# Optimization experiments

Hardware: AMD Instinct MI355X
Metric: run time of the kernel (lower is better)

## Reference

```python
import jax, jax.numpy as jnp
import numpy as np

D = 1024; H = 16; K = 64; BK = 32; FFN = 4096; LORA = 48; CHUNK = 64
THETA_CLIP = float(np.pi / 2)
THETA_INIT = float(np.pi / 16)


def layernorm(x, g, b, eps=1e-6):
    m = x.mean(-1, keepdims=True)
    v = ((x - m) ** 2).mean(-1, keepdims=True)
    return (x - m) * jax.lax.rsqrt(v + eps) * g + b


def setup_inputs() -> dict:
    key = jax.random.key(0)
    ks = jax.random.split(key, 24)
    w = lambda k, s: jax.random.normal(k, s, jnp.float32) * 0.02
    return {
        "x": jax.random.normal(ks[0], (4, 2048, D), jnp.float32),
        "Wq": w(ks[1], (D, D)), "bq": jnp.zeros((D,), jnp.float32),
        "Wk": w(ks[2], (D, D)), "bk": jnp.zeros((D,), jnp.float32),
        "Wv": w(ks[3], (D, D)), "bv": jnp.zeros((D,), jnp.float32),
        "Wo": w(ks[4], (D, D)), "bo": jnp.zeros((D,), jnp.float32),
        "n1g": jnp.ones((D,), jnp.float32), "n1b": jnp.zeros((D,), jnp.float32),
        "n2g": jnp.ones((D,), jnp.float32), "n2b": jnp.zeros((D,), jnp.float32),
        "theta_base": jax.random.uniform(ks[5], (H, BK), jnp.float32, -THETA_INIT, THETA_INIT),
        "theta_w1": w(ks[6], (D, LORA)),
        "theta_w2": jax.random.uniform(ks[7], (LORA, H * BK), jnp.float32, -0.01, 0.01),
        "lambda_base": jax.random.uniform(ks[8], (H, BK), jnp.float32, 0.5, 6.0),
        "eta": jax.random.normal(ks[9], (H, BK), jnp.float32) * 0.1,
        "Wf1": w(ks[10], (D, FFN)), "bf1": jnp.zeros((FFN,), jnp.float32),
        "Wf2": w(ks[11], (FFN, D)), "bf2": jnp.zeros((D,), jnp.float32),
    }


def _forward(x, Wq, bq, Wk, bk, Wv, bv, Wo, bo, n1g, n1b, n2g, n2b,
             theta_base, theta_w1, theta_w2, lambda_base, eta, Wf1, bf1, Wf2, bf2):
    B, T, _ = x.shape
    NC = T // CHUNK
    xn = layernorm(x, n1g, n1b)
    # projections -> (B, H, T, K)
    q = (xn @ Wq + bq).reshape(B, T, H, K).transpose(0, 2, 1, 3)
    k = (xn @ Wk + bk).reshape(B, T, H, K).transpose(0, 2, 1, 3)
    v = (xn @ Wv + bv).reshape(B, T, H, K).transpose(0, 2, 1, 3)
    phi_k = jnp.where(k > 0, k + 1.0, jnp.exp(k))  # elu(k) + 1
    qp = q.reshape(B, H, T, BK, 2)
    kp = phi_k.reshape(B, H, T, BK, 2)
    q_c = jax.lax.complex(qp[..., 0], qp[..., 1])  # (B,H,T,BK) complex64
    k_c = jax.lax.complex(kp[..., 0], kp[..., 1])
    # data-dependent rotation angles via LoRA
    lora = jnp.tanh(xn @ theta_w1) @ theta_w2  # (B,T,H*BK)
    theta = theta_base[None, None] + lora.reshape(B, T, H, BK)
    theta = jnp.clip(theta, -THETA_CLIP, THETA_CLIP).transpose(0, 2, 1, 3)  # (B,H,T,BK)
    lam = lambda_base[None, :, None, :] + eta[None, :, None, :] * theta ** 2
    log_z = jax.lax.complex(-lam, theta)  # complex log-decay per step

    def chunks(a):  # (B,H,T,...) -> (NC,B,H,CHUNK,...)
        return jnp.moveaxis(a.reshape(B, H, NC, CHUNK, *a.shape[3:]), 2, 0)

    tril = jnp.tril(jnp.ones((CHUNK, CHUNK), bool))[None, None, :, :, None]

    def step(c, inputs):
        lz, kc, qc, vf = inputs  # (B,H,tc,BK)x3, (B,H,tc,K)
        cumlog = jnp.cumsum(lz, axis=2)
        diff = cumlog[:, :, :, None, :] - cumlog[:, :, None, :, :]  # (B,H,tc,tc,BK)
        real = jnp.where(tril, diff.real, -60.0)
        A = jnp.where(tril, jnp.exp(jax.lax.complex(real, diff.imag)),
                      jnp.zeros((), jnp.complex64))
        scaled_k = A * kc[:, :, None, :, :]
        S_intra = jnp.einsum('bhtsk,bhsv->bhtkv', scaled_k, vf.astype(jnp.complex64))
        decay = jnp.exp(cumlog)
        S_total = decay[..., None] * c[:, :, None] + S_intra  # (B,H,tc,BK,K)
        y = jnp.einsum('bhtk,bhtkv->bhtv', jnp.conj(qc), S_total).real
        return S_total[:, :, -1], y

    c0 = jnp.zeros((B, H, BK, K), jnp.complex64)
    _, ys = jax.lax.scan(step, c0, (chunks(log_z), chunks(k_c), chunks(q_c), chunks(v)))
    out = jnp.moveaxis(ys, 0, 2).reshape(B, H, T, K)
    attn = out.transpose(0, 2, 1, 3).reshape(B, T, D) @ Wo + bo
    x1 = x + attn
    h = layernorm(x1, n2g, n2b)
    return x1 + jax.nn.gelu(h @ Wf1 + bf1) @ Wf2 + bf2


def reference(x, Wq, bq, Wk, bk, Wv, bv, Wo, bo, n1g, n1b, n2g, n2b,
              theta_base, theta_w1, theta_w2, lambda_base, eta, Wf1, bf1, Wf2, bf2):
    return _forward(x, Wq, bq, Wk, bk, Wv, bv, Wo, bo, n1g, n1b, n2g, n2b,
                    theta_base, theta_w1, theta_w2, lambda_base, eta, Wf1, bf1, Wf2, bf2)
```

## Files before the change

### kernel.cpp

```cpp
#include <hip/hip_runtime.h>


#define QS 3328

typedef __bf16 bf16x8 __attribute__((ext_vector_type(8)));
typedef float f32x4 __attribute__((ext_vector_type(4)));

__device__ __forceinline__ unsigned short f2bf(float f) {
  unsigned int u = __builtin_bit_cast(unsigned int, f);
  u += 0x7FFFu + ((u >> 16) & 1u);
  return (unsigned short)(u >> 16);
}
__device__ __forceinline__ float bf2f(unsigned short u) {
  unsigned int x = ((unsigned int)u) << 16;
  return __builtin_bit_cast(float, x);
}
__device__ __forceinline__ unsigned int pack2(float a, float b) {
  return (unsigned int)f2bf(a) | ((unsigned int)f2bf(b) << 16);
}

__device__ __forceinline__ void gload_lds16(const void* g, void* l) {
  __builtin_amdgcn_global_load_lds((const __attribute__((address_space(1))) void*)g,
                                   (__attribute__((address_space(3))) void*)l, 16, 0, 0);
}

__device__ __forceinline__ float gelu_tanh(float v) {
  const float z = 0.7978845608028654f * fmaf(0.044715f * v * v, v, v);
  const float e = __expf(2.f * z);
  return 0.5f * v * (2.f - 2.f / (1.f + e));
}

__global__ void fill_kernel(float* p, float v, int n) {
  int i = blockIdx.x * 256 + threadIdx.x;
  if (i < n) p[i] = v;
}

__global__ __launch_bounds__(256) void ln_kernel(
    const float* __restrict__ x, const float* __restrict__ g,
    const float* __restrict__ b, unsigned short* __restrict__ out) {
  const int row = blockIdx.x, tid = threadIdx.x;
  float4 v = ((const float4*)(x + (size_t)row * 1024))[tid];
  float s = v.x + v.y + v.z + v.w;
  float sq = v.x * v.x + v.y * v.y + v.z * v.z + v.w * v.w;
#pragma unroll
  for (int o = 32; o > 0; o >>= 1) { s += __shfl_xor(s, o); sq += __shfl_xor(sq, o); }
  __shared__ float red[8];
  const int wid = tid >> 6;
  if ((tid & 63) == 0) { red[wid] = s; red[4 + wid] = sq; }
  __syncthreads();
  s = red[0] + red[1] + red[2] + red[3];
  sq = red[4] + red[5] + red[6] + red[7];
  const float mean = s * (1.f / 1024.f);
  const float var = sq * (1.f / 1024.f) - mean * mean;
  const float rstd = rsqrtf(var + 1e-6f);
  float4 gv = ((const float4*)g)[tid];
  float4 bvv = ((const float4*)b)[tid];
  ushort4 o4;
  o4.x = f2bf((v.x - mean) * rstd * gv.x + bvv.x);
  o4.y = f2bf((v.y - mean) * rstd * gv.y + bvv.y);
  o4.z = f2bf((v.z - mean) * rstd * gv.z + bvv.z);
  o4.w = f2bf((v.w - mean) * rstd * gv.w + bvv.w);
  *(ushort4*)(out + (size_t)row * 1024 + tid * 4) = o4;
}

__global__ __launch_bounds__(256) void transpose_bf16(
    const float* __restrict__ src, unsigned short* __restrict__ dst, int K, int N) {
  __shared__ float tile[32][33];
  const int n0 = blockIdx.x * 32, k0 = blockIdx.y * 32;
  const int tx = threadIdx.x, ty = threadIdx.y;
#pragma unroll
  for (int j = 0; j < 32; j += 8) tile[tx][ty + j] = src[(size_t)(k0 + ty + j) * N + n0 + tx];
  __syncthreads();
#pragma unroll
  for (int j = 0; j < 32; j += 8)
    dst[(size_t)(n0 + ty + j) * K + k0 + tx] = f2bf(tile[ty + j][tx]);
}

__global__ __launch_bounds__(256) void prep_wcat(
    const float* __restrict__ Wq, const float* __restrict__ Wk,
    const float* __restrict__ Wv, const float* __restrict__ tw1,
    unsigned short* __restrict__ dst) {
  __shared__ float tile[32][33];
  const int r0 = blockIdx.x * 32, c0 = blockIdx.y * 32;
  const int tx = threadIdx.x, ty = threadIdx.y;
  const int r = r0 + tx;
#pragma unroll
  for (int j = 0; j < 32; j += 8) {
    const int c = c0 + ty + j;
    float v;
    if (r < 1024) v = Wq[(size_t)c * 1024 + r];
    else if (r < 2048) v = Wk[(size_t)c * 1024 + (r - 1024)];
    else if (r < 3072) v = Wv[(size_t)c * 1024 + (r - 2048)];
    else if (r < 3120) v = tw1[(size_t)c * 48 + (r - 3072)];
    else v = 0.f;
    tile[tx][ty + j] = v;
  }
  __syncthreads();
#pragma unroll
  for (int j = 0; j < 32; j += 8)
    dst[(size_t)(r0 + ty + j) * 1024 + c0 + tx] = f2bf(tile[ty + j][tx]);
}

__global__ void biascat_kernel(const float* bq, const float* bk, const float* bv, float* dst) {
  int i = blockIdx.x * 256 + threadIdx.x;
  if (i >= QS) return;
  float v = 0.f;
  if (i < 1024) v = bq[i];
  else if (i < 2048) v = bk[i - 1024];
  else if (i < 3072) v = bv[i - 2048];
  dst[i] = v;
}

template <int MODE>
__global__ __launch_bounds__(256) void gemm_kernel(
    const unsigned short* __restrict__ A, const unsigned short* __restrict__ BT,
    const float* __restrict__ bias, const float* __restrict__ res,
    void* __restrict__ out, int N, int Kd) {
  __shared__ unsigned short As[128 * 64];
  __shared__ unsigned short Bs[128 * 64];
  const int nwg = gridDim.x * gridDim.y;
  int d = blockIdx.y * gridDim.x + blockIdx.x;
  d = (d & 7) * (nwg >> 3) + (d >> 3);
  const int n0 = (d % gridDim.x) * 128, m0 = (d / gridDim.x) * 128;

  const int tid = threadIdx.x, wv = tid >> 6, ln = tid & 63;
  const int wm = wv >> 1, wn = wv & 1;
  const int l15 = ln & 15, hi4 = ln >> 4;
  const int rbase = wv * 8 + (ln >> 3);
  const int kgofs = ((ln & 7) ^ ((ln >> 3) & 7)) * 8;

  f32x4 acc[4][4] = {};
  for (int k0 = 0; k0 < Kd; k0 += 64) {
#pragma unroll
    for (int jj = 0; jj < 4; ++jj) {
      gload_lds16(A + (size_t)(m0 + jj * 32 + rbase) * Kd + k0 + kgofs,
                  (char*)As + (jj * 256 + wv * 64) * 16);
      gload_lds16(BT + (size_t)(n0 + jj * 32 + rbase) * Kd + k0 + kgofs,
                  (char*)Bs + (jj * 256 + wv * 64) * 16);
    }
    __syncthreads();
#pragma unroll
    for (int kk = 0; kk < 64; kk += 32) {
      const int kg = (kk >> 3) + hi4;
      bf16x8 av[4], bv[4];
#pragma unroll
      for (int f = 0; f < 4; ++f) {
        const int ra = wm * 64 + f * 16 + l15;
        const int rb2 = wn * 64 + f * 16 + l15;
        av[f] = *(const bf16x8*)&As[(ra * 8 + (kg ^ (ra & 7))) * 8];
        bv[f] = *(const bf16x8*)&Bs[(rb2 * 8 + (kg ^ (rb2 & 7))) * 8];
      }
#pragma unroll
      for (int fm = 0; fm < 4; ++fm)
#pragma unroll
        for (int fn = 0; fn < 4; ++fn)
          acc[fm][fn] = __builtin_amdgcn_mfma_f32_16x16x32_bf16(av[fm], bv[fn], acc[fm][fn], 0, 0, 0);
    }
    __syncthreads();
  }
  const int rb = hi4 * 4;
#pragma unroll
  for (int fm = 0; fm < 4; ++fm) {
#pragma unroll
    for (int fn = 0; fn < 4; ++fn) {
      const int row = m0 + wm * 64 + fm * 16 + rb;
      const int col = n0 + wn * 64 + fn * 16 + l15;
      const float bval = bias[col];
#pragma unroll
      for (int r = 0; r < 4; ++r) {
        float v = acc[fm][fn][r] + bval;
        const size_t oi = (size_t)(row + r) * N + col;
        if constexpr (MODE == 1) v += res[oi];
        ((float*)out)[oi] = v;
      }
    }
  }
}

template <int MODE>
__global__ __launch_bounds__(512, 2) void gemm8p_kernel(
    const unsigned short* __restrict__ A, const unsigned short* __restrict__ BT,
    const float* __restrict__ bias, void* __restrict__ out,
    int N, int Kstride, int Klen) {
  __shared__ __align__(16) unsigned short SA[2][2][8192];
  __shared__ __align__(16) unsigned short SB[2][2][8192];
  const int nwg = gridDim.x * gridDim.y;
  int d = blockIdx.y * gridDim.x + blockIdx.x;
  d = (d & 7) * (nwg >> 3) + (d >> 3);
  const int n0 = (d % gridDim.x) * 256, m0 = (d / gridDim.x) * 256;
  const int koff = blockIdx.z * Klen;

  const int tid = threadIdx.x, wv = tid >> 6, ln = tid & 63;
  const int wm = wv >> 2, wn = wv & 3;
  const int l15 = ln & 15, hi4 = ln >> 4;

  const unsigned short* Abase = A + (size_t)m0 * Kstride + koff;
  const unsigned short* Bbase = BT + (size_t)n0 * Kstride + koff;

  const int srow = ln >> 3;
  const int skg = (ln & 7) ^ srow;
  const unsigned short* ga00 = Abase + (size_t)((0 * 8 + wv) * 8 + srow) * Kstride + skg * 8;
  const unsigned short* ga01 = Abase + (size_t)((1 * 8 + wv) * 8 + srow) * Kstride + skg * 8;
  const unsigned short* ga10 = Abase + (size_t)(128 + (0 * 8 + wv) * 8 + srow) * Kstride + skg * 8;
  const unsigned short* ga11 = Abase + (size_t)(128 + (1 * 8 + wv) * 8 + srow) * Kstride + skg * 8;
  const unsigned short* gb00 = Bbase + (size_t)((0 * 8 + wv) * 8 + srow) * Kstride + skg * 8;
  const unsigned short* gb01 = Bbase + (size_t)((1 * 8 + wv) * 8 + srow) * Kstride + skg * 8;
  const unsigned short* gb10 = Bbase + (size_t)(128 + (0 * 8 + wv) * 8 + srow) * Kstride + skg * 8;
  const unsigned short* gb11 = Bbase + (size_t)(128 + (1 * 8 + wv) * 8 + srow) * Kstride + skg * 8;

  auto STA = [&](int pbuf) {
    gload_lds16(ga00, (char*)SA + pbuf * 32768 + wv * 1024);
    gload_lds16(ga01, (char*)SA + pbuf * 32768 + (8 + wv) * 1024);
    gload_lds16(ga10, (char*)SA + pbuf * 32768 + 16384 + wv * 1024);
    gload_lds16(ga11, (char*)SA + pbuf * 32768 + 16384 + (8 + wv) * 1024);
    ga00 += 64; ga01 += 64; ga10 += 64; ga11 += 64;
  };
  auto STB = [&](int pbuf) {
    gload_lds16(gb00, (char*)SB + pbuf * 32768 + wv * 1024);
    gload_lds16(gb01, (char*)SB + pbuf * 32768 + (8 + wv) * 1024);
    gload_lds16(gb10, (char*)SB + pbuf * 32768 + 16384 + wv * 1024);
    gload_lds16(gb11, (char*)SB + pbuf * 32768 + 16384 + (8 + wv) * 1024);
    gb00 += 64; gb01 += 64; gb10 += 64; gb11 += 64;
  };

  const int x7 = l15 & 7;
  const char* aA0 = (const char*)SA + wm * 16384 + l15 * 128 + ((hi4 ^ x7) * 16);
  const char* aA1 = (const char*)SA + wm * 16384 + l15 * 128 + (((4 + hi4) ^ x7) * 16);
  const char* aB0 = (const char*)SB + (wn >> 1) * 16384 + (wn & 1) * 8192 + l15 * 128 + ((hi4 ^ x7) * 16);
  const char* aB1 = (const char*)SB + (wn >> 1) * 16384 + (wn & 1) * 8192 + l15 * 128 + (((4 + hi4) ^ x7) * 16);

  f32x4 acc[8][4] = {};
  const int nt = Klen >> 6;

  STA(0);
  STB(0);
  STA(1);
  asm volatile("s_waitcnt vmcnt(4)" ::: "memory");
  __builtin_amdgcn_s_barrier();

#define GTILE(P, T)                                                            \
  {                                                                            \
    if ((T) + 1 < nt) STB((P) ^ 1);                                            \
    bf16x8 bfr0[4], bfr1[4];                                                   \
    _Pragma("unroll")                                                          \
    for (int fn = 0; fn < 4; ++fn) {                                           \
      bfr0[fn] = *(const bf16x8*)(aB0 + (P) * 32768 + fn * 2048);              \
      bfr1[fn] = *(const bf16x8*)(aB1 + (P) * 32768 + fn * 2048);              \
    }                                                                          \
    _Pragma("unroll")                                                          \
    for (int q = 0; q < 8; ++q) {                                              \
      bf16x8 a0 = *(const bf16x8*)(aA0 + (P) * 32768 + q * 2048);              \
      bf16x8 a1 = *(const bf16x8*)(aA1 + (P) * 32768 + q * 2048);              \
      __builtin_amdgcn_s_setprio(1);                                           \
      _Pragma("unroll")                                                        \
      for (int fn = 0; fn < 4; ++fn) {                                         \
        acc[q][fn] = __builtin_amdgcn_mfma_f32_16x16x32_bf16(a0, bfr0[fn],     \
                                                             acc[q][fn], 0, 0, 0); \
        acc[q][fn] = __builtin_amdgcn_mfma_f32_16x16x32_bf16(a1, bfr1[fn],     \
                                                             acc[q][fn], 0, 0, 0); \
      }                                                                        \
      __builtin_amdgcn_s_setprio(0);                                           \
    }                                                                          \
    __builtin_amdgcn_s_barrier();                                              \
    if ((T) + 2 < nt) STA(P);                                                  \
    if ((T) + 1 < nt) {                                                        \
      if ((T) + 2 < nt) asm volatile("s_waitcnt vmcnt(4)" ::: "memory");       \
      else              asm volatile("s_waitcnt vmcnt(0)" ::: "memory");       \
      __builtin_amdgcn_s_barrier();                                            \
    }                                                                          \
  }

  for (int t = 0; t < nt; t += 2) {
    GTILE(0, t);
    GTILE(1, t + 1);
  }
#undef GTILE

#pragma unroll
  for (int fm = 0; fm < 8; ++fm) {
#pragma unroll
    for (int fn = 0; fn < 4; ++fn) {
      const int row = m0 + wm * 128 + fm * 16 + hi4 * 4;
      const int col = n0 + wn * 64 + fn * 16 + l15;
      float bval = 0.f;
      if constexpr (MODE != 4) bval = bias[col];
#pragma unroll
      for (int r = 0; r < 4; ++r) {
        const float v = acc[fm][fn][r] + bval;
        const size_t oi = (size_t)(row + r) * N + col;
        if constexpr (MODE == 2) {
          ((unsigned short*)out)[oi] = f2bf(gelu_tanh(v));
        } else if constexpr (MODE == 3) {
          ((unsigned short*)out)[oi] = f2bf(v);
        } else {
          ((float*)out)[(size_t)blockIdx.z * 8192 * 1024 + oi] = v;
        }
      }
    }
  }
}

__global__ __launch_bounds__(256) void reduce2_kernel(
    const float* __restrict__ p0, const float* __restrict__ p1,
    const float* __restrict__ bias, const float* __restrict__ res,
    float* __restrict__ out) {
  const size_t i = ((size_t)blockIdx.x * 256 + threadIdx.x) * 4;
  float4 a = *(const float4*)&p0[i];
  float4 b = *(const float4*)&p1[i];
  float4 r = *(const float4*)&res[i];
  float4 bv = *(const float4*)&bias[i & 1023];
  float4 o;
  o.x = a.x + b.x + r.x + bv.x;
  o.y = a.y + b.y + r.y + bv.y;
  o.z = a.z + b.z + r.z + bv.z;
  o.w = a.w + b.w + r.w + bv.w;
  *(float4*)&out[i] = o;
}

__global__ __launch_bounds__(256) void lora2_kernel(
    const unsigned short* __restrict__ qkv, const float* __restrict__ w2,
    const float* __restrict__ tbase, float* __restrict__ theta) {
  __shared__ float lt[8][48];
  const int m0 = blockIdx.x * 32;
  const int tid = threadIdx.x;
  const int col = tid * 2;
  const float tb0 = tbase[col], tb1 = tbase[col + 1];
  for (int grp = 0; grp < 4; ++grp) {
    const int mg = m0 + grp * 8;
    __syncthreads();
    for (int idx = tid; idx < 384; idx += 256) {
      const int tok = idx / 48, jj = idx % 48;
      lt[tok][jj] = tanhf(bf2f(qkv[(size_t)(mg + tok) * QS + 3072 + jj]));
    }
    __syncthreads();
    float a0[8], a1[8];
#pragma unroll
    for (int tok = 0; tok < 8; ++tok) { a0[tok] = tb0; a1[tok] = tb1; }
    for (int jj = 0; jj < 48; ++jj) {
      const float2 w = *(const float2*)&w2[(size_t)jj * 512 + col];
#pragma unroll
      for (int tok = 0; tok < 8; ++tok) {
        const float l = lt[tok][jj];
        a0[tok] = fmaf(l, w.x, a0[tok]);
        a1[tok] = fmaf(l, w.y, a1[tok]);
      }
    }
    const float CL = 1.5707963267948966f;
#pragma unroll
    for (int tok = 0; tok < 8; ++tok) {
      float c0 = fminf(fmaxf(a0[tok], -CL), CL);
      float c1 = fminf(fmaxf(a1[tok], -CL), CL);
      *(float2*)&theta[(size_t)(mg + tok) * 512 + col] = make_float2(c0, c1);
    }
  }
}

__global__ __launch_bounds__(256) void attn_intra(
    const unsigned short* __restrict__ qkv, const float* __restrict__ theta,
    const float* __restrict__ lamb, const float* __restrict__ eta,
    float* __restrict__ yi, unsigned short* __restrict__ QG,
    unsigned short* __restrict__ TCG, float* __restrict__ Dg) {
  const int c = blockIdx.x, bh = blockIdx.y;
  const int b = bh >> 4, h = bh & 15;
  const int tid = threadIdx.x, wv = tid >> 6, lane = tid & 63;
  const int sc = c * 4 + wv;
  const int cid = bh * 128 + sc;
  const int mw = b * 2048 + sc * 16;

  __shared__ unsigned short QDm[4][16][64];
  __shared__ unsigned short KDm[4][16][64];
  __shared__ unsigned short KdET[4][64][32];
  __shared__ unsigned short VT[4][64][32];
  __shared__ unsigned short Gs[4][16][32];

  {
    unsigned int* kz = (unsigned int*)&KdET[wv][0][0];
    unsigned int* vz = (unsigned int*)&VT[wv][0][0];
    for (int idx = lane; idx < 512; idx += 64) {
      const int r = idx >> 3, p = (idx & 7) + 8;
      kz[r * 16 + p] = 0; vz[r * 16 + p] = 0;
    }
    unsigned int* gz = (unsigned int*)&Gs[wv][0][0];
    for (int idx = lane; idx < 128; idx += 64) {
      const int r = idx >> 3, p = (idx & 7) + 8;
      gz[r * 16 + p] = 0;
    }
  }
  for (int ss = 0; ss < 16; ++ss)
    VT[wv][lane][ss] = qkv[(size_t)(mw + ss) * QS + 2048 + h * 64 + lane];

  const int bk = lane & 31, th = lane >> 5;
  const float lb = lamb[h * 32 + bk], et = eta[h * 32 + bk];
  float L[8], Th[8], qr[8], qi[8], kr[8], ki[8];
  float runL = 0.f, runT = 0.f;
#pragma unroll
  for (int i = 0; i < 8; ++i) {
    const size_t m = (size_t)(mw + th * 8 + i);
    const float tv = theta[m * 512 + h * 32 + bk];
    const float lam = fmaf(et * tv, tv, lb);
    runL += lam; L[i] = runL;
    runT += tv;  Th[i] = runT;
    const unsigned int qp = *(const unsigned int*)&qkv[m * QS + h * 64 + 2 * bk];
    const unsigned int kp = *(const unsigned int*)&qkv[m * QS + 1024 + h * 64 + 2 * bk];
    qr[i] = bf2f((unsigned short)(qp & 0xFFFF)); qi[i] = bf2f((unsigned short)(qp >> 16));
    const float kx = bf2f((unsigned short)(kp & 0xFFFF));
    const float ky = bf2f((unsigned short)(kp >> 16));
    kr[i] = kx > 0.f ? kx + 1.f : __expf(kx);
    ki[i] = ky > 0.f ? ky + 1.f : __expf(ky);
  }
  const float oL = __shfl_xor(runL, 32), oT = __shfl_xor(runT, 32);
  const float Lm = th ? oL : runL;
  const float Tm = th ? oT : runT;
  const float Ltot = runL + oL, Ttot = runT + oT;
  const float Lbase = th ? oL : 0.f, Tbase = th ? oT : 0.f;
  float Es, Ec; __sincosf(Tm, &Es, &Ec);
  const float Ee = __expf(-Lm);
  const float Er = Ee * Ec, Ei = Ee * Es;
  float Fs, Fc; __sincosf(Ttot - Tm, &Fs, &Fc);
  const float Fe = __expf(-(Ltot - Lm));
  const float Fr = Fe * Fc, Fi = Fe * Fs;
  if (th == 0) {
    float Ds, Dc; __sincosf(Ttot, &Ds, &Dc);
    const float De = __expf(-Ltot);
    *(float2*)&Dg[((size_t)cid * 32 + bk) * 2] = make_float2(De * Dc, De * Ds);
  }
  unsigned int* qd32 = (unsigned int*)&QDm[wv][0][0];
  unsigned int* kd32 = (unsigned int*)&KDm[wv][0][0];
#pragma unroll
  for (int i = 0; i < 8; ++i) {
    const int t = th * 8 + i;
    const float Lg = Lbase + L[i], Tg = Tbase + Th[i];
    const float dm = __expf(-(Lg - Lm));
    float sn, cs; __sincosf(Tg - Tm, &sn, &cs);
    const float qmr = dm * (qr[i] * cs + qi[i] * sn);
    const float qmi = dm * (qr[i] * sn - qi[i] * cs);
    const float rd = 1.f / dm;
    const float kmr = rd * (kr[i] * cs + ki[i] * sn);
    const float kmi = rd * (ki[i] * cs - kr[i] * sn);
    const int sidx = (t * 32 + bk) ^ ((t & 7) << 2);
    qd32[sidx] = pack2(qmr, qmi);
    kd32[sidx] = pack2(kmr, -kmi);
    ((unsigned int*)QG)[(size_t)cid * 512 + t * 32 + bk] =
        pack2(qmr * Er - qmi * Ei, qmr * Ei + qmi * Er);
    const float er = kmr * Fr - kmi * Fi;
    const float ei = kmr * Fi + kmi * Fr;
    KdET[wv][bk][t] = f2bf(er);
    KdET[wv][32 + bk][t] = f2bf(ei);
  }

  const int l15 = lane & 15, hi = lane >> 4;
  const char* qb = (const char*)&QDm[wv][0][0];
  const char* kb = (const char*)&KDm[wv][0][0];
  f32x4 z = {};
  f32x4 g = z;
  {
    bf16x8 a0 = *(const bf16x8*)(qb + l15 * 128 + ((16 * hi) ^ ((l15 & 7) << 4)));
    bf16x8 b0 = *(const bf16x8*)(kb + l15 * 128 + ((16 * hi) ^ ((l15 & 7) << 4)));
    bf16x8 a1 = *(const bf16x8*)(qb + l15 * 128 + ((64 + 16 * hi) ^ ((l15 & 7) << 4)));
    bf16x8 b1 = *(const bf16x8*)(kb + l15 * 128 + ((64 + 16 * hi) ^ ((l15 & 7) << 4)));
    g = __builtin_amdgcn_mfma_f32_16x16x32_bf16(a0, b0, g, 0, 0, 0);
    g = __builtin_amdgcn_mfma_f32_16x16x32_bf16(a1, b1, g, 0, 0, 0);
  }
#pragma unroll
  for (int r = 0; r < 4; ++r) {
    const float gv = (l15 <= 4 * hi + r) ? g[r] : 0.f;
    Gs[wv][4 * hi + r][l15] = f2bf(gv);
  }
  const char* gsb = (const char*)&Gs[wv][0][0];
  const char* vtb = (const char*)&VT[wv][0][0];
  bf16x8 aG = *(const bf16x8*)(gsb + l15 * 64 + 16 * hi);
#pragma unroll
  for (int nt = 0; nt < 4; ++nt) {
    bf16x8 bV = *(const bf16x8*)(vtb + (nt * 16 + l15) * 64 + 16 * hi);
    f32x4 y = __builtin_amdgcn_mfma_f32_16x16x32_bf16(aG, bV, z, 0, 0, 0);
#pragma unroll
    for (int r = 0; r < 4; ++r)
      yi[(size_t)cid * 1024 + (4 * hi + r) * 64 + nt * 16 + l15] = y[r];
  }
  const char* keb = (const char*)&KdET[wv][0][0];
#pragma unroll
  for (int mt = 0; mt < 4; ++mt) {
    bf16x8 aT = *(const bf16x8*)(keb + (mt * 16 + l15) * 64 + 16 * hi);
#pragma unroll
    for (int nt = 0; nt < 4; ++nt) {
      bf16x8 bV = *(const bf16x8*)(vtb + (nt * 16 + l15) * 64 + 16 * hi);
      f32x4 t4 = __builtin_amdgcn_mfma_f32_16x16x32_bf16(aT, bV, z, 0, 0, 0);
#pragma unroll
      for (int r = 0; r < 4; ++r)
        TCG[(size_t)cid * 4096 + (mt * 16 + 4 * hi + r) * 64 + nt * 16 + l15] = f2bf(t4[r]);
    }
  }
}

__global__ __launch_bounds__(256) void scanB_kernel(
    const unsigned short* __restrict__ TCG, const float* __restrict__ Dg,
    unsigned int* __restrict__ CPACK) {
  const int bh = blockIdx.x & 63, g = blockIdx.x >> 6;
  const int tid = threadIdx.x;
  const int v = g * 8 + (tid >> 5), bk = tid & 31;
  const size_t base = (size_t)bh * 128;
  float Cr = 0.f, Ci = 0.f;
  float trx[4], tix[4]; float2 dx[4];
  auto LOADQ = [&](int c0, float* tr, float* ti, float2* dd) {
#pragma unroll
    for (int u = 0; u < 4; ++u) {
      const size_t cid = base + c0 + u;
      tr[u] = bf2f(TCG[cid * 4096 + bk * 64 + v]);
      ti[u] = bf2f(TCG[cid * 4096 + (32 + bk) * 64 + v]);
      dd[u] = *(const float2*)&Dg[(cid * 32 + bk) * 2];
    }
  };
  LOADQ(0, trx, tix, dx);
  for (int c0 = 0; c0 < 128; c0 += 4) {
    float tra[4], tia[4]; float2 da[4];
#pragma unroll
    for (int u = 0; u < 4; ++u) { tra[u] = trx[u]; tia[u] = tix[u]; da[u] = dx[u]; }
    if (c0 + 4 < 128) LOADQ(c0 + 4, trx, tix, dx);
#pragma unroll
    for (int u = 0; u < 4; ++u) {
      CPACK[(base + c0 + u) * 2048 + v * 32 + bk] = pack2(Cr, -Ci);
      const float nr = fmaf(da[u].x, Cr, fmaf(-da[u].y, Ci, tra[u]));
      const float ni = fmaf(da[u].x, Ci, fmaf(da[u].y, Cr, tia[u]));
      Cr = nr; Ci = ni;
    }
  }
}

__global__ __launch_bounds__(256) void attn_cross(
    const float* __restrict__ yi, const unsigned short* __restrict__ QG,
    const unsigned int* __restrict__ CPACK, unsigned short* __restrict__ attn) {
  const int c = blockIdx.x, bh = blockIdx.y;
  const int b = bh >> 4, h = bh & 15;
  const int tid = threadIdx.x, wv = tid >> 6, lane = tid & 63;
  const int sc = c * 4 + wv, cid = bh * 128 + sc;
  const int mw = b * 2048 + sc * 16;
  __shared__ unsigned short Cp[4][64][64];
  __shared__ unsigned short Qs[4][16][64];
  unsigned int* cp32 = (unsigned int*)&Cp[wv][0][0];
  const unsigned int* cg = CPACK + (size_t)cid * 2048;
  for (int ii = 0; ii < 32; ++ii) {
    const int flat = ii * 64 + lane;
    const int row = flat >> 5, col = flat & 31;
    cp32[(row * 32 + col) ^ ((row & 7) << 2)] = cg[flat];
  }
  unsigned int* qs32 = (unsigned int*)&Qs[wv][0][0];
  const unsigned int* qg = (const unsigned int*)QG + (size_t)cid * 512;
  for (int ii = 0; ii < 8; ++ii) {
    const int flat = ii * 64 + lane;
    const int row = flat >> 5, col = flat & 31;
    qs32[(row * 32 + col) ^ ((row & 7) << 2)] = qg[flat];
  }
  const int l15 = lane & 15, hi = lane >> 4;
  const char* qb = (const char*)&Qs[wv][0][0];
  const char* cb = (const char*)&Cp[wv][0][0];
  bf16x8 a0 = *(const bf16x8*)(qb + l15 * 128 + ((16 * hi) ^ ((l15 & 7) << 4)));
  bf16x8 a1 = *(const bf16x8*)(qb + l15 * 128 + ((64 + 16 * hi) ^ ((l15 & 7) << 4)));
  f32x4 z = {};
#pragma unroll
  for (int nt = 0; nt < 4; ++nt) {
    const int vr = nt * 16 + l15;
    bf16x8 b0 = *(const bf16x8*)(cb + vr * 128 + ((16 * hi) ^ ((vr & 7) << 4)));
    bf16x8 b1 = *(const bf16x8*)(cb + vr * 128 + ((64 + 16 * hi) ^ ((vr & 7) << 4)));
    f32x4 y = __builtin_amdgcn_mfma_f32_16x16x32_bf16(a0, b0, z, 0, 0, 0);
    y = __builtin_amdgcn_mfma_f32_16x16x32_bf16(a1, b1, y, 0, 0, 0);
#pragma unroll
    for (int r = 0; r < 4; ++r) {
      const int t = 4 * hi + r;
      const float out = y[r] + yi[(size_t)cid * 1024 + t * 64 + vr];
      attn[(size_t)(mw + t) * 1024 + h * 64 + vr] = f2bf(out);
    }
  }
}

extern "C" void kernel_launch(void* const* d_in, const int* in_sizes, int n_in,
                              void* d_out, int out_size, void* d_ws, size_t ws_size,
                              hipStream_t stream) {
  const float* x   = (const float*)d_in[0];
  const float* Wq  = (const float*)d_in[1];
  const float* bq  = (const float*)d_in[2];
  const float* Wk  = (const float*)d_in[3];
  const float* bk_ = (const float*)d_in[4];
  const float* Wv  = (const float*)d_in[5];
  const float* bv  = (const float*)d_in[6];
  const float* Wo  = (const float*)d_in[7];
  const float* bo  = (const float*)d_in[8];
  const float* n1g = (const float*)d_in[9];
  const float* n1b = (const float*)d_in[10];
  const float* n2g = (const float*)d_in[11];
  const float* n2b = (const float*)d_in[12];
  const float* thb = (const float*)d_in[13];
  const float* tw1 = (const float*)d_in[14];
  const float* tw2 = (const float*)d_in[15];
  const float* lamb= (const float*)d_in[16];
  const float* eta = (const float*)d_in[17];
  const float* Wf1 = (const float*)d_in[18];
  const float* bf1 = (const float*)d_in[19];
  const float* Wf2 = (const float*)d_in[20];
  const float* bf2 = (const float*)d_in[21];

  char* ws = (char*)d_ws;
  size_t off = 0;
  auto alloc = [&](size_t bytes) {
    size_t r = off;
    off += (bytes + 255) & ~(size_t)255;
    return r;
  };
  unsigned short* WCAT = (unsigned short*)(ws + alloc((size_t)QS * 1024 * 2));
  unsigned short* WOT  = (unsigned short*)(ws + alloc(1024ull * 1024 * 2));
  unsigned short* WF1T = (unsigned short*)(ws + alloc(4096ull * 1024 * 2));
  unsigned short* WF2T = (unsigned short*)(ws + alloc(1024ull * 4096 * 2));
  float* BIASC = (float*)(ws + alloc((size_t)QS * 4));
  unsigned short* XN = (unsigned short*)(ws + alloc(8192ull * 1024 * 2));
  char* QKVbase = ws + alloc(8192ull * 4096 * 2);
  unsigned short* QKV = (unsigned short*)QKVbase;
  unsigned int* CPACK = (unsigned int*)QKVbase;
  unsigned short* GBUF = (unsigned short*)QKVbase;
  float* THETA = (float*)(ws + alloc(8192ull * 512 * 4));
  unsigned short* ATTN = (unsigned short*)THETA;
  float* YI = (float*)(ws + alloc(8192ull * 1024 * 4));
  float* X1 = YI;
  unsigned short* QG = (unsigned short*)(ws + alloc(8192ull * 1024 * 2));
  char* TCGbase = ws + alloc(8192ull * 4096 * 2);
  unsigned short* TCG = (unsigned short*)TCGbase;
  float* PART = (float*)TCGbase;
  float* DG = (float*)(ws + alloc(8192ull * 32 * 2 * 4));

  if (ws_size < off) {
    fill_kernel<<<dim3((out_size + 255) / 256), dim3(256), 0, stream>>>((float*)d_out, 12345.0f, out_size);
    return;
  }

  const dim3 b256(256), b32x8(32, 8), b512(512);

  prep_wcat<<<dim3(104, 32), b32x8, 0, stream>>>(Wq, Wk, Wv, tw1, WCAT);
  transpose_bf16<<<dim3(32, 32), b32x8, 0, stream>>>(Wo, WOT, 1024, 1024);
  transpose_bf16<<<dim3(128, 32), b32x8, 0, stream>>>(Wf1, WF1T, 1024, 4096);
  transpose_bf16<<<dim3(32, 128), b32x8, 0, stream>>>(Wf2, WF2T, 4096, 1024);
  biascat_kernel<<<dim3(13), b256, 0, stream>>>(bq, bk_, bv, BIASC);

  ln_kernel<<<dim3(8192), b256, 0, stream>>>(x, n1g, n1b, XN);
  gemm8p_kernel<3><<<dim3(13, 32), b512, 0, stream>>>(XN, WCAT, BIASC, QKV, QS, 1024, 1024);
  lora2_kernel<<<dim3(256), b256, 0, stream>>>(QKV, tw2, thb, THETA);
  attn_intra<<<dim3(32, 64), b256, 0, stream>>>(QKV, THETA, lamb, eta, YI, QG, TCG, DG);
  scanB_kernel<<<dim3(512), b256, 0, stream>>>(TCG, DG, CPACK);
  attn_cross<<<dim3(32, 64), b256, 0, stream>>>(YI, QG, CPACK, ATTN);
  gemm_kernel<1><<<dim3(8, 64), b256, 0, stream>>>(ATTN, WOT, bo, x, X1, 1024, 1024);
  ln_kernel<<<dim3(8192), b256, 0, stream>>>(X1, n2g, n2b, XN);
  gemm8p_kernel<2><<<dim3(16, 32), b512, 0, stream>>>(XN, WF1T, bf1, GBUF, 4096, 1024, 1024);
  gemm8p_kernel<4><<<dim3(4, 32, 2), b512, 0, stream>>>(GBUF, WF2T, nullptr, PART, 1024, 4096, 2048);
  reduce2_kernel<<<dim3(8192), b256, 0, stream>>>(PART, PART + 8192ull * 1024, bf2, X1, (float*)d_out);
}
```

Baseline: 483.8 us.

## Add 256x128 pipelined GEMM with fused residual; drop split-K and reduce pass

```diff
diff --git a/kernel.cpp b/kernel.cpp
--- a/kernel.cpp
+++ b/kernel.cpp
@@ -112,72 +112,6 @@
 }
 
 template <int MODE>
-__global__ __launch_bounds__(256) void gemm_kernel(
-    const unsigned short* __restrict__ A, const unsigned short* __restrict__ BT,
-    const float* __restrict__ bias, const float* __restrict__ res,
-    void* __restrict__ out, int N, int Kd) {
-  __shared__ unsigned short As[128 * 64];
-  __shared__ unsigned short Bs[128 * 64];
-  const int nwg = gridDim.x * gridDim.y;
-  int d = blockIdx.y * gridDim.x + blockIdx.x;
-  d = (d & 7) * (nwg >> 3) + (d >> 3);
-  const int n0 = (d % gridDim.x) * 128, m0 = (d / gridDim.x) * 128;
-
-  const int tid = threadIdx.x, wv = tid >> 6, ln = tid & 63;
-  const int wm = wv >> 1, wn = wv & 1;
-  const int l15 = ln & 15, hi4 = ln >> 4;
-  const int rbase = wv * 8 + (ln >> 3);
-  const int kgofs = ((ln & 7) ^ ((ln >> 3) & 7)) * 8;
-
-  f32x4 acc[4][4] = {};
-  for (int k0 = 0; k0 < Kd; k0 += 64) {
-#pragma unroll
-    for (int jj = 0; jj < 4; ++jj) {
-      gload_lds16(A + (size_t)(m0 + jj * 32 + rbase) * Kd + k0 + kgofs,
-                  (char*)As + (jj * 256 + wv * 64) * 16);
-      gload_lds16(BT + (size_t)(n0 + jj * 32 + rbase) * Kd + k0 + kgofs,
-                  (char*)Bs + (jj * 256 + wv * 64) * 16);
-    }
-    __syncthreads();
-#pragma unroll
-    for (int kk = 0; kk < 64; kk += 32) {
-      const int kg = (kk >> 3) + hi4;
-      bf16x8 av[4], bv[4];
-#pragma unroll
-      for (int f = 0; f < 4; ++f) {
-        const int ra = wm * 64 + f * 16 + l15;
-        const int rb2 = wn * 64 + f * 16 + l15;
-        av[f] = *(const bf16x8*)&As[(ra * 8 + (kg ^ (ra & 7))) * 8];
-        bv[f] = *(const bf16x8*)&Bs[(rb2 * 8 + (kg ^ (rb2 & 7))) * 8];
-      }
-#pragma unroll
-      for (int fm = 0; fm < 4; ++fm)
-#pragma unroll
-        for (int fn = 0; fn < 4; ++fn)
-          acc[fm][fn] = __builtin_amdgcn_mfma_f32_16x16x32_bf16(av[fm], bv[fn], acc[fm][fn], 0, 0, 0);
-    }
-    __syncthreads();
-  }
-  const int rb = hi4 * 4;
-#pragma unroll
-  for (int fm = 0; fm < 4; ++fm) {
-#pragma unroll
-    for (int fn = 0; fn < 4; ++fn) {
-      const int row = m0 + wm * 64 + fm * 16 + rb;
-      const int col = n0 + wn * 64 + fn * 16 + l15;
-      const float bval = bias[col];
-#pragma unroll
-      for (int r = 0; r < 4; ++r) {
-        float v = acc[fm][fn][r] + bval;
-        const size_t oi = (size_t)(row + r) * N + col;
-        if constexpr (MODE == 1) v += res[oi];
-        ((float*)out)[oi] = v;
-      }
-    }
-  }
-}
-
-template <int MODE>
 __global__ __launch_bounds__(512, 2) void gemm8p_kernel(
     const unsigned short* __restrict__ A, const unsigned short* __restrict__ BT,
     const float* __restrict__ bias, void* __restrict__ out,
@@ -188,14 +122,13 @@
   int d = blockIdx.y * gridDim.x + blockIdx.x;
   d = (d & 7) * (nwg >> 3) + (d >> 3);
   const int n0 = (d % gridDim.x) * 256, m0 = (d / gridDim.x) * 256;
-  const int koff = blockIdx.z * Klen;
 
   const int tid = threadIdx.x, wv = tid >> 6, ln = tid & 63;
   const int wm = wv >> 2, wn = wv & 3;
   const int l15 = ln & 15, hi4 = ln >> 4;
 
-  const unsigned short* Abase = A + (size_t)m0 * Kstride + koff;
-  const unsigned short* Bbase = BT + (size_t)n0 * Kstride + koff;
+  const unsigned short* Abase = A + (size_t)m0 * Kstride;
+  const unsigned short* Bbase = BT + (size_t)n0 * Kstride;
 
   const int srow = ln >> 3;
   const int skg = (ln & 7) ^ srow;
@@ -282,39 +215,128 @@
     for (int fn = 0; fn < 4; ++fn) {
       const int row = m0 + wm * 128 + fm * 16 + hi4 * 4;
       const int col = n0 + wn * 64 + fn * 16 + l15;
-      float bval = 0.f;
-      if constexpr (MODE != 4) bval = bias[col];
+      const float bval = bias[col];
 #pragma unroll
       for (int r = 0; r < 4; ++r) {
         const float v = acc[fm][fn][r] + bval;
         const size_t oi = (size_t)(row + r) * N + col;
         if constexpr (MODE == 2) {
           ((unsigned short*)out)[oi] = f2bf(gelu_tanh(v));
-        } else if constexpr (MODE == 3) {
+        } else {
           ((unsigned short*)out)[oi] = f2bf(v);
-        } else {
-          ((float*)out)[(size_t)blockIdx.z * 8192 * 1024 + oi] = v;
         }
       }
     }
   }
 }
 
-__global__ __launch_bounds__(256) void reduce2_kernel(
-    const float* __restrict__ p0, const float* __restrict__ p1,
+__global__ __launch_bounds__(512, 2) void gemm8pn_kernel(
+    const unsigned short* __restrict__ A, const unsigned short* __restrict__ BT,
     const float* __restrict__ bias, const float* __restrict__ res,
-    float* __restrict__ out) {
-  const size_t i = ((size_t)blockIdx.x * 256 + threadIdx.x) * 4;
-  float4 a = *(const float4*)&p0[i];
-  float4 b = *(const float4*)&p1[i];
-  float4 r = *(const float4*)&res[i];
-  float4 bv = *(const float4*)&bias[i & 1023];
-  float4 o;
-  o.x = a.x + b.x + r.x + bv.x;
-  o.y = a.y + b.y + r.y + bv.y;
-  o.z = a.z + b.z + r.z + bv.z;
-  o.w = a.w + b.w + r.w + bv.w;
-  *(float4*)&out[i] = o;
+    float* __restrict__ out, int N, int Kstride, int Klen) {
+  __shared__ __align__(16) unsigned short SA[2][2][8192];
+  __shared__ __align__(16) unsigned short SB[2][8192];
+  const int nwg = gridDim.x * gridDim.y;
+  int d = blockIdx.y * gridDim.x + blockIdx.x;
+  d = (d & 7) * (nwg >> 3) + (d >> 3);
+  const int n0 = (d % gridDim.x) * 128, m0 = (d / gridDim.x) * 256;
+
+  const int tid = threadIdx.x, wv = tid >> 6, ln = tid & 63;
+  const int wm = wv >> 1, wn = wv & 1;
+  const int l15 = ln & 15, hi4 = ln >> 4;
+
+  const unsigned short* Abase = A + (size_t)m0 * Kstride;
+  const unsigned short* Bbase = BT + (size_t)n0 * Kstride;
+
+  const int srow = ln >> 3;
+  const int skg = (ln & 7) ^ srow;
+  const unsigned short* ga00 = Abase + (size_t)((0 * 8 + wv) * 8 + srow) * Kstride + skg * 8;
+  const unsigned short* ga01 = Abase + (size_t)((1 * 8 + wv) * 8 + srow) * Kstride + skg * 8;
+  const unsigned short* ga10 = Abase + (size_t)(128 + (0 * 8 + wv) * 8 + srow) * Kstride + skg * 8;
+  const unsigned short* ga11 = Abase + (size_t)(128 + (1 * 8 + wv) * 8 + srow) * Kstride + skg * 8;
+  const unsigned short* gb0 = Bbase + (size_t)((0 * 8 + wv) * 8 + srow) * Kstride + skg * 8;
+  const unsigned short* gb1 = Bbase + (size_t)((1 * 8 + wv) * 8 + srow) * Kstride + skg * 8;
+
+  auto STA = [&](int pbuf) {
+    gload_lds16(ga00, (char*)SA + pbuf * 32768 + wv * 1024);
+    gload_lds16(ga01, (char*)SA + pbuf * 32768 + (8 + wv) * 1024);
+    gload_lds16(ga10, (char*)SA + pbuf * 32768 + 16384 + wv * 1024);
+    gload_lds16(ga11, (char*)SA + pbuf * 32768 + 16384 + (8 + wv) * 1024);
+    ga00 += 64; ga01 += 64; ga10 += 64; ga11 += 64;
+  };
+  auto STB = [&](int pbuf) {
+    gload_lds16(gb0, (char*)SB + pbuf * 16384 + wv * 1024);
+    gload_lds16(gb1, (char*)SB + pbuf * 16384 + (8 + wv) * 1024);
+    gb0 += 64; gb1 += 64;
+  };
+
+  const int x7 = l15 & 7;
+  const char* aA0 = (const char*)SA + (wm >> 1) * 16384 + (wm & 1) * 8192 + l15 * 128 + ((hi4 ^ x7) * 16);
+  const char* aA1 = (const char*)SA + (wm >> 1) * 16384 + (wm & 1) * 8192 + l15 * 128 + (((4 + hi4) ^ x7) * 16);
+  const char* aB0 = (const char*)SB + wn * 8192 + l15 * 128 + ((hi4 ^ x7) * 16);
+  const char* aB1 = (const char*)SB + wn * 8192 + l15 * 128 + (((4 + hi4) ^ x7) * 16);
+
+  f32x4 acc[4][4] = {};
+  const int nt = Klen >> 6;
+
+  STA(0);
+  STB(0);
+  STA(1);
+  asm volatile("s_waitcnt vmcnt(4)" ::: "memory");
+  __builtin_amdgcn_s_barrier();
+
+#define GTILEN(P, T)                                                           \
+  {                                                                            \
+    if ((T) + 1 < nt) STB((P) ^ 1);                                            \
+    bf16x8 bfr0[4], bfr1[4];                                                   \
+    _Pragma("unroll")                                                          \
+    for (int fn = 0; fn < 4; ++fn) {                                           \
+      bfr0[fn] = *(const bf16x8*)(aB0 + (P) * 16384 + fn * 2048);              \
+      bfr1[fn] = *(const bf16x8*)(aB1 + (P) * 16384 + fn * 2048);              \
+    }                                                                          \
+    _Pragma("unroll")                                                          \
+    for (int q = 0; q < 4; ++q) {                                              \
+      bf16x8 a0 = *(const bf16x8*)(aA0 + (P) * 32768 + q * 2048);              \
+      bf16x8 a1 = *(const bf16x8*)(aA1 + (P) * 32768 + q * 2048);              \
+      __builtin_amdgcn_s_setprio(1);                                           \
+      _Pragma("unroll")                                                        \
+      for (int fn = 0; fn < 4; ++fn) {                                         \
+        acc[q][fn] = __builtin_amdgcn_mfma_f32_16x16x32_bf16(a0, bfr0[fn],     \
+                                                             acc[q][fn], 0, 0, 0); \
+        acc[q][fn] = __builtin_amdgcn_mfma_f32_16x16x32_bf16(a1, bfr1[fn],     \
+                                                             acc[q][fn], 0, 0, 0); \
+      }                                                                        \
+      __builtin_amdgcn_s_setprio(0);                                           \
+    }                                                                          \
+    __builtin_amdgcn_s_barrier();                                              \
+    if ((T) + 2 < nt) STA(P);                                                  \
+    if ((T) + 1 < nt) {                                                        \
+      if ((T) + 2 < nt) asm volatile("s_waitcnt vmcnt(4)" ::: "memory");       \
+      else              asm volatile("s_waitcnt vmcnt(0)" ::: "memory");       \
+      __builtin_amdgcn_s_barrier();                                            \
+    }                                                                          \
+  }
+
+  for (int t = 0; t < nt; t += 2) {
+    GTILEN(0, t);
+    GTILEN(1, t + 1);
+  }
+#undef GTILEN
+
+#pragma unroll
+  for (int fm = 0; fm < 4; ++fm) {
+#pragma unroll
+    for (int fn = 0; fn < 4; ++fn) {
+      const int row = m0 + wm * 64 + fm * 16 + hi4 * 4;
+      const int col = n0 + wn * 64 + fn * 16 + l15;
+      const float bval = bias[col];
+#pragma unroll
+      for (int r = 0; r < 4; ++r) {
+        const size_t oi = (size_t)(row + r) * N + col;
+        out[oi] = acc[fm][fn][r] + bval + res[oi];
+      }
+    }
+  }
 }
 
 __global__ __launch_bounds__(256) void lora2_kernel(
@@ -497,7 +519,7 @@
     unsigned int* __restrict__ CPACK) {
   const int bh = blockIdx.x & 63, g = blockIdx.x >> 6;
   const int tid = threadIdx.x;
-  const int v = g * 8 + (tid >> 5), bk = tid & 31;
+  const int v = tid & 63, bk = g * 4 + (tid >> 6);
   const size_t base = (size_t)bh * 128;
   float Cr = 0.f, Ci = 0.f;
   float trx[4], tix[4]; float2 dx[4];
@@ -518,7 +540,7 @@
     if (c0 + 4 < 128) LOADQ(c0 + 4, trx, tix, dx);
 #pragma unroll
     for (int u = 0; u < 4; ++u) {
-      CPACK[(base + c0 + u) * 2048 + v * 32 + bk] = pack2(Cr, -Ci);
+      CPACK[(base + c0 + u) * 2048 + bk * 64 + v] = pack2(Cr, -Ci);
       const float nr = fmaf(da[u].x, Cr, fmaf(-da[u].y, Ci, tra[u]));
       const float ni = fmaf(da[u].x, Ci, fmaf(da[u].y, Cr, tia[u]));
       Cr = nr; Ci = ni;
@@ -538,10 +560,8 @@
   __shared__ unsigned short Qs[4][16][64];
   unsigned int* cp32 = (unsigned int*)&Cp[wv][0][0];
   const unsigned int* cg = CPACK + (size_t)cid * 2048;
-  for (int ii = 0; ii < 32; ++ii) {
-    const int flat = ii * 64 + lane;
-    const int row = flat >> 5, col = flat & 31;
-    cp32[(row * 32 + col) ^ ((row & 7) << 2)] = cg[flat];
+  for (int bkq = 0; bkq < 32; ++bkq) {
+    cp32[(lane * 32 + bkq) ^ ((lane & 7) << 2)] = cg[bkq * 64 + lane];
   }
   unsigned int* qs32 = (unsigned int*)&Qs[wv][0][0];
   const unsigned int* qg = (const unsigned int*)QG + (size_t)cid * 512;
@@ -620,9 +640,7 @@
   float* YI = (float*)(ws + alloc(8192ull * 1024 * 4));
   float* X1 = YI;
   unsigned short* QG = (unsigned short*)(ws + alloc(8192ull * 1024 * 2));
-  char* TCGbase = ws + alloc(8192ull * 4096 * 2);
-  unsigned short* TCG = (unsigned short*)TCGbase;
-  float* PART = (float*)TCGbase;
+  unsigned short* TCG = (unsigned short*)(ws + alloc(8192ull * 4096 * 2));
   float* DG = (float*)(ws + alloc(8192ull * 32 * 2 * 4));
 
   if (ws_size < off) {
@@ -644,9 +662,8 @@
   attn_intra<<<dim3(32, 64), b256, 0, stream>>>(QKV, THETA, lamb, eta, YI, QG, TCG, DG);
   scanB_kernel<<<dim3(512), b256, 0, stream>>>(TCG, DG, CPACK);
   attn_cross<<<dim3(32, 64), b256, 0, stream>>>(YI, QG, CPACK, ATTN);
-  gemm_kernel<1><<<dim3(8, 64), b256, 0, stream>>>(ATTN, WOT, bo, x, X1, 1024, 1024);
+  gemm8pn_kernel<<<dim3(8, 32), b512, 0, stream>>>(ATTN, WOT, bo, x, X1, 1024, 1024, 1024);
   ln_kernel<<<dim3(8192), b256, 0, stream>>>(X1, n2g, n2b, XN);
   gemm8p_kernel<2><<<dim3(16, 32), b512, 0, stream>>>(XN, WF1T, bf1, GBUF, 4096, 1024, 1024);
-  gemm8p_kernel<4><<<dim3(4, 32, 2), b512, 0, stream>>>(GBUF, WF2T, nullptr, PART, 1024, 4096, 2048);
-  reduce2_kernel<<<dim3(8192), b256, 0, stream>>>(PART, PART + 8192ull * 1024, bf2, X1, (float*)d_out);
-}
+  gemm8pn_kernel<<<dim3(8, 32), b512, 0, stream>>>(GBUF, WF2T, bf2, X1, (float*)d_out, 1024, 4096, 4096);
+}
```

Result: faster. 436.3 us (-9.8%).
